# Optimization experiments

Hardware: AMD Instinct MI355X
Metric: run time of the kernel (lower is better)

The kernel has to match this reference:

```python
import jax, jax.numpy as jnp
import numpy as np

EMBED = 256
HEADS = 8
LEVELS = 4
POINTS = 4
HD = EMBED // HEADS  # 32
SHAPES = [(100, 100), (50, 50), (25, 25), (13, 13)]  # (H, W) per level
NV = sum(h * w for h, w in SHAPES)  # 13294
BS = 2


def _lin_params(k, fan_in, fan_out):
    s = 1.0 / np.sqrt(fan_in)
    kw, kb = jax.random.split(k)
    W = jax.random.uniform(kw, (fan_in, fan_out), jnp.float32, -s, s)
    b = jax.random.uniform(kb, (fan_out,), jnp.float32, -s, s)
    return W, b


def setup_inputs():
    key = jax.random.key(0)
    ks = jax.random.split(key, 10)
    inp = {
        "query": jax.random.normal(ks[0], (BS, NV, EMBED), jnp.float32),
        "key": jax.random.normal(ks[1], (BS, NV, EMBED), jnp.float32),
        "value": jax.random.normal(ks[2], (BS, NV, EMBED), jnp.float32),
        "query_pos": jax.random.normal(ks[3], (BS, NV, EMBED), jnp.float32),
        "reference_points": jax.random.uniform(ks[4], (BS, NV, LEVELS, 2), jnp.float32),
        "spatial_shapes": jnp.array(SHAPES, jnp.int32),
        "level_start_index": jnp.array(np.cumsum([0] + [h * w for h, w in SHAPES[:-1]]), jnp.int32),
        "key_padding_mask": jnp.zeros((BS, NV), bool),
    }
    inp["W_value"], inp["b_value"] = _lin_params(ks[5], EMBED, EMBED)
    inp["W_off"], inp["b_off"] = _lin_params(ks[6], EMBED, HEADS * LEVELS * POINTS * 2)
    inp["W_attn"], inp["b_attn"] = _lin_params(ks[7], EMBED, HEADS * LEVELS * POINTS)
    inp["W_out"], inp["b_out"] = _lin_params(ks[8], EMBED, EMBED)
    inp["W_ffn"], inp["b_ffn"] = _lin_params(ks[9], EMBED, EMBED)
    return inp


def _bilinear(v, x, y, H, W):
    # v: (bs, heads, H*W, hd); x, y: (bs, heads, n) pixel coords (align_corners=False)
    # zero padding outside the feature map (matches torch grid_sample padding_mode='zeros')
    x0 = jnp.floor(x)
    y0 = jnp.floor(y)
    lx = x - x0
    ly = y - y0
    x0 = x0.astype(jnp.int32)
    y0 = y0.astype(jnp.int32)

    def g(xi, yi):
        valid = ((xi >= 0) & (xi < W) & (yi >= 0) & (yi < H)).astype(v.dtype)
        idx = jnp.clip(yi, 0, H - 1) * W + jnp.clip(xi, 0, W - 1)
        return jnp.take_along_axis(v, idx[..., None], axis=2) * valid[..., None]

    return (g(x0, y0) * ((1 - lx) * (1 - ly))[..., None]
            + g(x0 + 1, y0) * (lx * (1 - ly))[..., None]
            + g(x0, y0 + 1) * ((1 - lx) * ly)[..., None]
            + g(x0 + 1, y0 + 1) * (lx * ly)[..., None])


def _forward(query, key, value, query_pos, reference_points, shapes, starts,
             key_padding_mask, W_value, b_value, W_off, b_off, W_attn, b_attn,
             W_out, b_out, W_ffn, b_ffn):
    bs, nq, _ = query.shape
    identity = query  # residual taken BEFORE adding positional encoding (mmcv semantics)
    q = query + query_pos
    v = value @ W_value + b_value
    v = jnp.where(key_padding_mask[..., None], 0.0, v).reshape(bs, -1, HEADS, HD)
    off = (q @ W_off + b_off).reshape(bs, nq, HEADS, LEVELS, POINTS, 2)
    aw = jax.nn.softmax((q @ W_attn + b_attn).reshape(bs, nq, HEADS, LEVELS * POINTS), axis=-1)
    aw = aw.reshape(bs, nq, HEADS, LEVELS, POINTS)
    # offset normalizer is (W, H) per level
    wh = jnp.array([[w, h] for h, w in shapes], jnp.float32)
    loc = reference_points[:, :, None, :, None, :] + off / wh[None, None, None, :, None, :]
    out = jnp.zeros((bs, HEADS, nq, HD), q.dtype)
    for l, (H, W) in enumerate(shapes):
        s = starts[l]
        vl = v[:, s:s + H * W].transpose(0, 2, 1, 3)  # (bs, heads, H*W, hd)
        x = (loc[:, :, :, l, :, 0] * W - 0.5).transpose(0, 2, 1, 3).reshape(bs, HEADS, nq * POINTS)
        y = (loc[:, :, :, l, :, 1] * H - 0.5).transpose(0, 2, 1, 3).reshape(bs, HEADS, nq * POINTS)
        smp = _bilinear(vl, x, y, H, W).reshape(bs, HEADS, nq, POINTS, HD)
        wl = aw[:, :, :, l].transpose(0, 2, 1, 3)  # (bs, heads, nq, P)
        out = out + jnp.sum(smp * wl[..., None], axis=3)
    out = out.transpose(0, 2, 1, 3).reshape(bs, nq, EMBED)
    out = out @ W_out + b_out + identity
    return out @ W_ffn + b_ffn


def reference(query, key, value, query_pos, reference_points, spatial_shapes,
              level_start_index, key_padding_mask, W_value, b_value, W_off, b_off,
              W_attn, b_attn, W_out, b_out, W_ffn, b_ffn):
    # spatial shapes / level starts are structural metadata -> treat as static ints
    shapes = [tuple(int(x) for x in r) for r in np.asarray(spatial_shapes)]
    starts = [int(x) for x in np.asarray(level_start_index)]
    return _forward(query, key, value, query_pos, reference_points, shapes, starts,
                    key_padding_mask, W_value, b_value, W_off, b_off, W_attn, b_attn,
                    W_out, b_out, W_ffn, b_ffn)
```

## Files before the change

kernel.cpp:

```cpp
#include <hip/hip_runtime.h>
#include <hip/hip_bf16.h>
#include <math.h>

#define NQ 13294
#define NV 13294
#define M_ROWS (2*NQ)
#define MP 26624

typedef __attribute__((ext_vector_type(8))) short bf16x8;
typedef __attribute__((ext_vector_type(4))) float f32x4;
typedef __attribute__((ext_vector_type(2))) float f32x2;

__device__ __forceinline__ float4 ld4(const float* p){ return *(const float4*)p; }
__device__ __forceinline__ float bfu_lo(unsigned int u){ return __uint_as_float(u << 16); }
__device__ __forceinline__ float bfu_hi(unsigned int u){ return __uint_as_float(u & 0xffff0000u); }
__device__ __forceinline__ f32x2 up2(unsigned int u){
  return (f32x2){__uint_as_float(u << 16), __uint_as_float(u & 0xffff0000u)};
}
__device__ __forceinline__ unsigned short f2bf(float f){
  unsigned int u = __float_as_uint(f);
  u += 0x7fffu + ((u >> 16) & 1u);
  return (unsigned short)(u >> 16);
}
__device__ __forceinline__ unsigned int pk2(float a, float b){
  return (unsigned int)f2bf(a) | ((unsigned int)f2bf(b) << 16);
}
__device__ __forceinline__ void gl_lds16(const unsigned short* g, unsigned short* l) {
  __builtin_amdgcn_global_load_lds(
      (const __attribute__((address_space(1))) unsigned int*)g,
      (__attribute__((address_space(3))) unsigned int*)l, 16, 0, 0);
}

__global__ __launch_bounds__(256) void prep_all(
    const float* __restrict__ value, const float* __restrict__ query,
    const float* __restrict__ qpos,
    unsigned short* __restrict__ val_bf, unsigned short* __restrict__ q_bf,
    const float* __restrict__ wv, const float* __restrict__ wo,
    const float* __restrict__ wa, const float* __restrict__ wu,
    const float* __restrict__ wf, unsigned short* __restrict__ wt)
{
  const int total = MP * 64;
  for (int i = blockIdx.x * 256 + threadIdx.x; i < total; i += gridDim.x * 256) {
    const int e = i * 4;
    ushort4 a = make_ushort4(0,0,0,0), b = make_ushort4(0,0,0,0);
    if (e < M_ROWS * 256) {
      float4 v4 = ld4(value + e);
      a = make_ushort4(f2bf(v4.x), f2bf(v4.y), f2bf(v4.z), f2bf(v4.w));
      float4 q4 = ld4(query + e);
      float4 p4 = ld4(qpos + e);
      b = make_ushort4(f2bf(q4.x+p4.x), f2bf(q4.y+p4.y), f2bf(q4.z+p4.z), f2bf(q4.w+p4.w));
    }
    *(ushort4*)(val_bf + e) = a;
    *(ushort4*)(q_bf   + e) = b;
  }
  for (int t = blockIdx.x * 256 + threadIdx.x; t < 294912; t += gridDim.x * 256) {
    const float* src; int Nn; int base;
    if      (t < 65536)  { src = wv; Nn = 256; base = 0; }
    else if (t < 131072) { src = wo; Nn = 256; base = 65536; }
    else if (t < 163840) { src = wa; Nn = 128; base = 131072; }
    else if (t < 229376) { src = wu; Nn = 256; base = 163840; }
    else                 { src = wf; Nn = 256; base = 229376; }
    const int local = t - base;
    const int n = local >> 8, k = local & 255;
    wt[t] = f2bf(src[k * Nn + n]);
  }
}

template<int NCOL, int OUT_MODE, bool ADD_RES>
__global__ __launch_bounds__(256) void gemm_gl(
    const unsigned short* __restrict__ A, const unsigned short* __restrict__ Bt,
    const float* __restrict__ biasA, const float* __restrict__ biasB,
    const float* __restrict__ RES, void* __restrict__ Cv, int N)
{
  __shared__ unsigned short lds[32768];

  const int nwg = 416 * NCOL;
  const int lin = blockIdx.x;
  const int swz = (lin & 7) * (nwg >> 3) + (lin >> 3);
  const int brow = (swz / NCOL) * 64;
  const int bcol = (swz % NCOL) * 64;

  const int tid  = threadIdx.x;
  const int wid  = tid >> 6, lane = tid & 63;
  const int wr   = wid >> 1, wc = wid & 1;
  const int fr   = lane & 15, fg = lane >> 4;

  {
    const int r0   = lane >> 3;
    const int slot = lane & 7;
    #pragma unroll
    for (int t = 0; t < 4; ++t) {
      #pragma unroll
      for (int c = 0; c < 2; ++c) {
        const int row = (wid * 2 + c) * 8 + r0;
        const int gsl = slot ^ (row & 7);
        gl_lds16(A  + (size_t)(brow + row) * 256 + t * 64 + (gsl << 3),
                 &lds[t * 4096 + (wid * 2 + c) * 512]);
        gl_lds16(Bt + (size_t)(bcol + row) * 256 + t * 64 + (gsl << 3),
                 &lds[16384 + t * 4096 + (wid * 2 + c) * 512]);
      }
    }
  }
  __syncthreads();

  f32x4 acc[2][2];
  #pragma unroll
  for (int m = 0; m < 2; ++m)
    #pragma unroll
    for (int n = 0; n < 2; ++n)
      acc[m][n] = (f32x4){0.f, 0.f, 0.f, 0.f};

  #pragma unroll
  for (int t = 0; t < 4; ++t) {
    const char* as = (const char*)&lds[t * 4096];
    const char* bs = (const char*)&lds[16384 + t * 4096];
    #pragma unroll
    for (int kk = 0; kk < 2; ++kk) {
      const int kb = kk * 64 + fg * 16;
      bf16x8 af[2], bfv[2];
      #pragma unroll
      for (int m = 0; m < 2; ++m) {
        const int r = wr * 32 + m * 16 + fr;
        af[m] = *(const bf16x8*)(as + r * 128 + (kb ^ ((r & 7) << 4)));
      }
      #pragma unroll
      for (int n = 0; n < 2; ++n) {
        const int r = wc * 32 + n * 16 + fr;
        bfv[n] = *(const bf16x8*)(bs + r * 128 + (kb ^ ((r & 7) << 4)));
      }
      #pragma unroll
      for (int m = 0; m < 2; ++m)
        #pragma unroll
        for (int n = 0; n < 2; ++n)
          acc[m][n] = __builtin_amdgcn_mfma_f32_16x16x32_bf16(af[m], bfv[n], acc[m][n], 0, 0, 0);
    }
  }

  __syncthreads();
  float* csh = (float*)lds;
  const int c0 = bcol + wc * 32 + fr;
  const int c1 = c0 + 16;
  const float bn0 = (c0 < 256) ? biasA[c0] : biasB[c0 - 256];
  const float bn1 = (c1 < 256) ? biasA[c1] : biasB[c1 - 256];
  #pragma unroll
  for (int m = 0; m < 2; ++m)
    #pragma unroll
    for (int j = 0; j < 4; ++j) {
      const int row = wr * 32 + m * 16 + fg * 4 + j;
      csh[row * 64 + wc * 32 + fr]      = acc[m][0][j] + bn0;
      csh[row * 64 + wc * 32 + 16 + fr] = acc[m][1][j] + bn1;
    }
  __syncthreads();
  #pragma unroll
  for (int i = 0; i < 4; ++i) {
    const int rl = i * 16 + (tid >> 4);
    const int gr = brow + rl;
    if (gr >= M_ROWS) continue;
    const int c4 = (tid & 15) * 4;
    float4 v = *(const float4*)&csh[rl * 64 + c4];
    if (ADD_RES) {
      float4 q = ld4(RES + (size_t)gr * 256 + bcol + c4);
      v.x += q.x; v.y += q.y; v.z += q.z; v.w += q.w;
    }
    if (OUT_MODE == 0) {
      *(float4*)&((float*)Cv)[(size_t)gr * N + bcol + c4] = v;
    } else if (OUT_MODE == 1) {
      ushort4 pk = make_ushort4(f2bf(v.x), f2bf(v.y), f2bf(v.z), f2bf(v.w));
      *(ushort4*)&((unsigned short*)Cv)[(size_t)gr * N + bcol + c4] = pk;
    } else {
      const int head = (bcol + c4) >> 5;
      const int ch   = c4 & 31;
      ushort4 pk = make_ushort4(f2bf(v.x), f2bf(v.y), f2bf(v.z), f2bf(v.w));
      *(ushort4*)&((unsigned short*)Cv)[((size_t)head * M_ROWS + gr) * 32 + ch] = pk;
    }
  }
}

__global__ __launch_bounds__(256) void msda5(
    const unsigned short* __restrict__ v, const unsigned short* __restrict__ oa,
    const float* __restrict__ ref, unsigned short* __restrict__ attout)
{
  constexpr int LW[4] = {100, 50, 25, 13};
  constexpr int LS[4] = {0, 10000, 12500, 13125};

  __shared__ int4   sidx[64][16];
  __shared__ float4 swt [64][16];

  const int bid   = blockIdx.x;
  const int h     = bid & 7;
  const int chunk = bid >> 3;
  const int tid   = threadIdx.x;
  const int qi    = tid >> 2;
  const int lq    = tid & 3;
  const int bq    = chunk * 64 + qi;
  const bool active = bq < M_ROWS;
  const int b     = (bq >= NQ) ? 1 : 0;
  const int pmask = qi & 7;

  if (active) {
    const int l = lq;
    const int W = LW[l];
    const float fD = (float)W;
    const unsigned short* oarow = oa + (size_t)bq * 384;

    uint2 lg = *(const uint2*)(oarow + 256 + h * 16 + l * 4);
    float g0 = bfu_lo(lg.x), g1 = bfu_hi(lg.x), g2 = bfu_lo(lg.y), g3 = bfu_hi(lg.y);
    float mx = fmaxf(fmaxf(g0, g1), fmaxf(g2, g3));
    mx = fmaxf(mx, __shfl_xor(mx, 1));
    mx = fmaxf(mx, __shfl_xor(mx, 2));
    float e0 = __expf(g0-mx), e1 = __expf(g1-mx), e2 = __expf(g2-mx), e3 = __expf(g3-mx);
    float s = e0 + e1 + e2 + e3;
    s += __shfl_xor(s, 1);
    s += __shfl_xor(s, 2);
    const float inv = 1.f / s;
    const float ee[4] = {e0*inv, e1*inv, e2*inv, e3*inv};

    uint4 ov = *(const uint4*)(oarow + h * 32 + l * 8);
    const float oxy[8] = {bfu_lo(ov.x), bfu_hi(ov.x), bfu_lo(ov.y), bfu_hi(ov.y),
                          bfu_lo(ov.z), bfu_hi(ov.z), bfu_lo(ov.w), bfu_hi(ov.w)};
    const float rx = ref[(size_t)bq * 8 + l * 2];
    const float ry = ref[(size_t)bq * 8 + l * 2 + 1];
    const int rowbase = b * NV + LS[l];

    #pragma unroll
    for (int j = 0; j < 4; ++j) {
      const float x = fmaf(rx, fD, oxy[2*j])   - 0.5f;
      const float y = fmaf(ry, fD, oxy[2*j+1]) - 0.5f;
      const float x0f = floorf(x), y0f = floorf(y);
      const float lx = x - x0f, ly = y - y0f;
      const int x0 = (int)x0f, y0 = (int)y0f;
      const int x1 = x0 + 1,  y1 = y0 + 1;
      const int cx0 = min(max(x0, 0), W - 1), cx1 = min(max(x1, 0), W - 1);
      const int cy0 = min(max(y0, 0), W - 1), cy1 = min(max(y1, 0), W - 1);
      const float f00 = (x0 >= 0 && x0 < W && y0 >= 0 && y0 < W) ? 1.f : 0.f;
      const float f10 = (x1 >= 0 && x1 < W && y0 >= 0 && y0 < W) ? 1.f : 0.f;
      const float f01 = (x0 >= 0 && x0 < W && y1 >= 0 && y1 < W) ? 1.f : 0.f;
      const float f11 = (x1 >= 0 && x1 < W && y1 >= 0 && y1 < W) ? 1.f : 0.f;
      const float wt = ee[j];
      const int pi = (l * 4 + j) ^ pmask;
      sidx[qi][pi] = make_int4((rowbase + cy0 * W + cx0) * 64,
                               (rowbase + cy0 * W + cx1) * 64,
                               (rowbase + cy1 * W + cx0) * 64,
                               (rowbase + cy1 * W + cx1) * 64);
      swt[qi][pi] = make_float4(wt * (1.f - lx) * (1.f - ly) * f00,
                                wt * lx * (1.f - ly) * f10,
                                wt * (1.f - lx) * ly * f01,
                                wt * lx * ly * f11);
    }
  }
  __syncthreads();

  if (active) {
    const char* vb = (const char*)v + (size_t)h * M_ROWS * 64 + lq * 16;
    f32x2 acc2[4];
    #pragma unroll
    for (int k = 0; k < 4; ++k) acc2[k] = (f32x2){0.f, 0.f};
    #pragma unroll
    for (int p = 0; p < 16; ++p) {
      const int4   ix = sidx[qi][p ^ pmask];
      const float4 w4 = swt[qi][p ^ pmask];
      uint4 c0 = *(const uint4*)(vb + ix.x);
      uint4 c1 = *(const uint4*)(vb + ix.y);
      uint4 c2 = *(const uint4*)(vb + ix.z);
      uint4 c3 = *(const uint4*)(vb + ix.w);
      const f32x2 w0 = (f32x2){w4.x, w4.x};
      const f32x2 w1 = (f32x2){w4.y, w4.y};
      const f32x2 w2 = (f32x2){w4.z, w4.z};
      const f32x2 w3 = (f32x2){w4.w, w4.w};
      acc2[0] = w0 * up2(c0.x) + acc2[0];
      acc2[1] = w0 * up2(c0.y) + acc2[1];
      acc2[2] = w0 * up2(c0.z) + acc2[2];
      acc2[3] = w0 * up2(c0.w) + acc2[3];
      acc2[0] = w1 * up2(c1.x) + acc2[0];
      acc2[1] = w1 * up2(c1.y) + acc2[1];
      acc2[2] = w1 * up2(c1.z) + acc2[2];
      acc2[3] = w1 * up2(c1.w) + acc2[3];
      acc2[0] = w2 * up2(c2.x) + acc2[0];
      acc2[1] = w2 * up2(c2.y) + acc2[1];
      acc2[2] = w2 * up2(c2.z) + acc2[2];
      acc2[3] = w2 * up2(c2.w) + acc2[3];
      acc2[0] = w3 * up2(c3.x) + acc2[0];
      acc2[1] = w3 * up2(c3.y) + acc2[1];
      acc2[2] = w3 * up2(c3.z) + acc2[2];
      acc2[3] = w3 * up2(c3.w) + acc2[3];
    }
    uint4 pk;
    pk.x = pk2(acc2[0][0], acc2[0][1]);
    pk.y = pk2(acc2[1][0], acc2[1][1]);
    pk.z = pk2(acc2[2][0], acc2[2][1]);
    pk.w = pk2(acc2[3][0], acc2[3][1]);
    *(uint4*)(attout + (size_t)bq * 256 + h * 32 + lq * 8) = pk;
  }
}

extern "C" void kernel_launch(void* const* d_in, const int* in_sizes, int n_in,
                              void* d_out, int out_size, void* d_ws, size_t ws_size,
                              hipStream_t stream) {
  const float* query  = (const float*)d_in[0];
  const float* value  = (const float*)d_in[2];
  const float* qpos   = (const float*)d_in[3];
  const float* refpts = (const float*)d_in[4];
  const float* W_value = (const float*)d_in[8];
  const float* b_value = (const float*)d_in[9];
  const float* W_off   = (const float*)d_in[10];
  const float* b_off   = (const float*)d_in[11];
  const float* W_attn  = (const float*)d_in[12];
  const float* b_attn  = (const float*)d_in[13];
  const float* W_out   = (const float*)d_in[14];
  const float* b_out   = (const float*)d_in[15];
  const float* W_ffn   = (const float*)d_in[16];
  const float* b_ffn   = (const float*)d_in[17];
  float* out = (float*)d_out;

  unsigned short* oa    = (unsigned short*)d_ws;
  unsigned short* vbuf2 = oa + (size_t)MP * 384;
  unsigned short* AB1   = vbuf2 + (size_t)8 * M_ROWS * 32;
  unsigned short* AB2   = AB1 + (size_t)MP * 256;
  unsigned short* wts   = AB2 + (size_t)MP * 256;
  unsigned short* wv_t  = wts;
  unsigned short* woa_t = wts + 65536;
  unsigned short* wu_t  = wts + 163840;
  unsigned short* wf_t  = wts + 229376;

  const dim3 blk(256);

  prep_all<<<dim3(2048), blk, 0, stream>>>(value, query, qpos, AB1, AB2,
      W_value, W_off, W_attn, W_out, W_ffn, wts);

  gemm_gl<4,2,false><<<dim3(1664), blk, 0, stream>>>(
      AB1, wv_t, b_value, b_value, nullptr, vbuf2, 256);
  gemm_gl<6,1,false><<<dim3(2496), blk, 0, stream>>>(
      AB2, woa_t, b_off, b_attn, nullptr, oa, 384);
  msda5<<<dim3(8 * 416), blk, 0, stream>>>(vbuf2, oa, refpts, AB1);
  gemm_gl<4,1,true><<<dim3(1664), blk, 0, stream>>>(
      AB1, wu_t, b_out, b_out, query, AB2, 256);
  gemm_gl<4,0,false><<<dim3(1664), blk, 0, stream>>>(
      AB2, wf_t, b_ffn, b_ffn, nullptr, (void*)out, 256);
}
```

Measured before the change: 123.2 us.

## Fetch bilinear x-neighbour pairs as one 32-byte row load in sampling kernel

The sampling kernel now uses 8 threads per query instead of 4. Each thread pair covers the two horizontally adjacent corners of a bilinear sample with a single contiguous 16-byte load per row, and edge cases are handled by clamping the x base to W-2 and remapping the corner weights. Per-query gathers drop from four scattered loads to two wider contiguous row segments, and partial sums are combined with a shuffle. The cost is twice as many blocks, half the threads idling at the store, and a new edge-weight remapping that must match zero padding exactly.

```diff
diff --git a/kernel.cpp b/kernel.cpp
--- a/kernel.cpp
+++ b/kernel.cpp
@@ -176,120 +176,115 @@
   }
 }
 
-__global__ __launch_bounds__(256) void msda5(
+__global__ __launch_bounds__(256) void msda6(
     const unsigned short* __restrict__ v, const unsigned short* __restrict__ oa,
     const float* __restrict__ ref, unsigned short* __restrict__ attout)
 {
   constexpr int LW[4] = {100, 50, 25, 13};
   constexpr int LS[4] = {0, 10000, 12500, 13125};
 
-  __shared__ int4   sidx[64][16];
-  __shared__ float4 swt [64][16];
+  __shared__ int2   sidx[32][17];
+  __shared__ float4 swt [32][17];
 
   const int bid   = blockIdx.x;
   const int h     = bid & 7;
   const int chunk = bid >> 3;
   const int tid   = threadIdx.x;
-  const int qi    = tid >> 2;
-  const int lq    = tid & 3;
-  const int bq    = chunk * 64 + qi;
+  const int q     = tid >> 3;
+  const int c     = tid & 7;
+  const int bq    = chunk * 32 + q;
   const bool active = bq < M_ROWS;
   const int b     = (bq >= NQ) ? 1 : 0;
-  const int pmask = qi & 7;
 
   if (active) {
-    const int l = lq;
+    const int l = c >> 1;
     const int W = LW[l];
     const float fD = (float)W;
     const unsigned short* oarow = oa + (size_t)bq * 384;
 
-    uint2 lg = *(const uint2*)(oarow + 256 + h * 16 + l * 4);
-    float g0 = bfu_lo(lg.x), g1 = bfu_hi(lg.x), g2 = bfu_lo(lg.y), g3 = bfu_hi(lg.y);
-    float mx = fmaxf(fmaxf(g0, g1), fmaxf(g2, g3));
+    unsigned int lgu = *(const unsigned int*)(oarow + 256 + h * 16 + c * 2);
+    float g0 = bfu_lo(lgu), g1 = bfu_hi(lgu);
+    float mx = fmaxf(g0, g1);
     mx = fmaxf(mx, __shfl_xor(mx, 1));
     mx = fmaxf(mx, __shfl_xor(mx, 2));
-    float e0 = __expf(g0-mx), e1 = __expf(g1-mx), e2 = __expf(g2-mx), e3 = __expf(g3-mx);
-    float s = e0 + e1 + e2 + e3;
+    mx = fmaxf(mx, __shfl_xor(mx, 4));
+    float e0 = __expf(g0 - mx), e1 = __expf(g1 - mx);
+    float s = e0 + e1;
     s += __shfl_xor(s, 1);
     s += __shfl_xor(s, 2);
+    s += __shfl_xor(s, 4);
     const float inv = 1.f / s;
-    const float ee[4] = {e0*inv, e1*inv, e2*inv, e3*inv};
-
-    uint4 ov = *(const uint4*)(oarow + h * 32 + l * 8);
-    const float oxy[8] = {bfu_lo(ov.x), bfu_hi(ov.x), bfu_lo(ov.y), bfu_hi(ov.y),
-                          bfu_lo(ov.z), bfu_hi(ov.z), bfu_lo(ov.w), bfu_hi(ov.w)};
+    const float wpt[2] = {e0 * inv, e1 * inv};
+
+    uint2 ou = *(const uint2*)(oarow + h * 32 + c * 4);
+    const float oxy[4] = {bfu_lo(ou.x), bfu_hi(ou.x), bfu_lo(ou.y), bfu_hi(ou.y)};
     const float rx = ref[(size_t)bq * 8 + l * 2];
     const float ry = ref[(size_t)bq * 8 + l * 2 + 1];
     const int rowbase = b * NV + LS[l];
 
     #pragma unroll
-    for (int j = 0; j < 4; ++j) {
+    for (int j = 0; j < 2; ++j) {
       const float x = fmaf(rx, fD, oxy[2*j])   - 0.5f;
       const float y = fmaf(ry, fD, oxy[2*j+1]) - 0.5f;
       const float x0f = floorf(x), y0f = floorf(y);
       const float lx = x - x0f, ly = y - y0f;
       const int x0 = (int)x0f, y0 = (int)y0f;
-      const int x1 = x0 + 1,  y1 = y0 + 1;
-      const int cx0 = min(max(x0, 0), W - 1), cx1 = min(max(x1, 0), W - 1);
+      const int y1 = y0 + 1;
+      const int xbase = min(max(x0, 0), W - 2);
+      const float wx0 = 1.f - lx, wx1 = lx;
+      const float we0 = (x0 == xbase     ? wx0 : 0.f) + (x0 == xbase - 1 ? wx1 : 0.f);
+      const float we1 = (x0 == xbase + 1 ? wx0 : 0.f) + (x0 == xbase     ? wx1 : 0.f);
       const int cy0 = min(max(y0, 0), W - 1), cy1 = min(max(y1, 0), W - 1);
-      const float f00 = (x0 >= 0 && x0 < W && y0 >= 0 && y0 < W) ? 1.f : 0.f;
-      const float f10 = (x1 >= 0 && x1 < W && y0 >= 0 && y0 < W) ? 1.f : 0.f;
-      const float f01 = (x0 >= 0 && x0 < W && y1 >= 0 && y1 < W) ? 1.f : 0.f;
-      const float f11 = (x1 >= 0 && x1 < W && y1 >= 0 && y1 < W) ? 1.f : 0.f;
-      const float wt = ee[j];
-      const int pi = (l * 4 + j) ^ pmask;
-      sidx[qi][pi] = make_int4((rowbase + cy0 * W + cx0) * 64,
-                               (rowbase + cy0 * W + cx1) * 64,
-                               (rowbase + cy1 * W + cx0) * 64,
-                               (rowbase + cy1 * W + cx1) * 64);
-      swt[qi][pi] = make_float4(wt * (1.f - lx) * (1.f - ly) * f00,
-                                wt * lx * (1.f - ly) * f10,
-                                wt * (1.f - lx) * ly * f01,
-                                wt * lx * ly * f11);
+      const float wy0 = (y0 >= 0 && y0 < W) ? (1.f - ly) : 0.f;
+      const float wy1 = (y1 >= 0 && y1 < W) ? ly : 0.f;
+      const float wt = wpt[j];
+      const int p = c * 2 + j;
+      sidx[q][p] = make_int2((rowbase + cy0 * W + xbase) * 64,
+                             (rowbase + cy1 * W + xbase) * 64);
+      swt[q][p] = make_float4(wt * wy0 * we0, wt * wy0 * we1,
+                              wt * wy1 * we0, wt * wy1 * we1);
     }
   }
   __syncthreads();
 
   if (active) {
-    const char* vb = (const char*)v + (size_t)h * M_ROWS * 64 + lq * 16;
+    const char* vb = (const char*)v + (size_t)h * M_ROWS * 64 + c * 16;
+    const int el = c >> 2;
     f32x2 acc2[4];
     #pragma unroll
     for (int k = 0; k < 4; ++k) acc2[k] = (f32x2){0.f, 0.f};
     #pragma unroll
     for (int p = 0; p < 16; ++p) {
-      const int4   ix = sidx[qi][p ^ pmask];
-      const float4 w4 = swt[qi][p ^ pmask];
-      uint4 c0 = *(const uint4*)(vb + ix.x);
-      uint4 c1 = *(const uint4*)(vb + ix.y);
-      uint4 c2 = *(const uint4*)(vb + ix.z);
-      uint4 c3 = *(const uint4*)(vb + ix.w);
-      const f32x2 w0 = (f32x2){w4.x, w4.x};
-      const f32x2 w1 = (f32x2){w4.y, w4.y};
-      const f32x2 w2 = (f32x2){w4.z, w4.z};
-      const f32x2 w3 = (f32x2){w4.w, w4.w};
-      acc2[0] = w0 * up2(c0.x) + acc2[0];
-      acc2[1] = w0 * up2(c0.y) + acc2[1];
-      acc2[2] = w0 * up2(c0.z) + acc2[2];
-      acc2[3] = w0 * up2(c0.w) + acc2[3];
-      acc2[0] = w1 * up2(c1.x) + acc2[0];
-      acc2[1] = w1 * up2(c1.y) + acc2[1];
-      acc2[2] = w1 * up2(c1.z) + acc2[2];
-      acc2[3] = w1 * up2(c1.w) + acc2[3];
-      acc2[0] = w2 * up2(c2.x) + acc2[0];
-      acc2[1] = w2 * up2(c2.y) + acc2[1];
-      acc2[2] = w2 * up2(c2.z) + acc2[2];
-      acc2[3] = w2 * up2(c2.w) + acc2[3];
-      acc2[0] = w3 * up2(c3.x) + acc2[0];
-      acc2[1] = w3 * up2(c3.y) + acc2[1];
-      acc2[2] = w3 * up2(c3.z) + acc2[2];
-      acc2[3] = w3 * up2(c3.w) + acc2[3];
-    }
-    uint4 pk;
-    pk.x = pk2(acc2[0][0], acc2[0][1]);
-    pk.y = pk2(acc2[1][0], acc2[1][1]);
-    pk.z = pk2(acc2[2][0], acc2[2][1]);
-    pk.w = pk2(acc2[3][0], acc2[3][1]);
-    *(uint4*)(attout + (size_t)bq * 256 + h * 32 + lq * 8) = pk;
+      const int2   ix = sidx[q][p];
+      const float4 w4 = swt[q][p];
+      uint4 r0 = *(const uint4*)(vb + ix.x);
+      uint4 r1 = *(const uint4*)(vb + ix.y);
+      const float wa = el ? w4.y : w4.x;
+      const float wb = el ? w4.w : w4.z;
+      const f32x2 wav = (f32x2){wa, wa};
+      const f32x2 wbv = (f32x2){wb, wb};
+      acc2[0] = wav * up2(r0.x) + acc2[0];
+      acc2[1] = wav * up2(r0.y) + acc2[1];
+      acc2[2] = wav * up2(r0.z) + acc2[2];
+      acc2[3] = wav * up2(r0.w) + acc2[3];
+      acc2[0] = wbv * up2(r1.x) + acc2[0];
+      acc2[1] = wbv * up2(r1.y) + acc2[1];
+      acc2[2] = wbv * up2(r1.z) + acc2[2];
+      acc2[3] = wbv * up2(r1.w) + acc2[3];
+    }
+    #pragma unroll
+    for (int k = 0; k < 4; ++k) {
+      acc2[k][0] += __shfl_xor(acc2[k][0], 4);
+      acc2[k][1] += __shfl_xor(acc2[k][1], 4);
+    }
+    if (c < 4) {
+      uint4 pk;
+      pk.x = pk2(acc2[0][0], acc2[0][1]);
+      pk.y = pk2(acc2[1][0], acc2[1][1]);
+      pk.z = pk2(acc2[2][0], acc2[2][1]);
+      pk.w = pk2(acc2[3][0], acc2[3][1]);
+      *(uint4*)(attout + (size_t)bq * 256 + h * 32 + c * 8) = pk;
+    }
   }
 }
 
@@ -331,7 +326,7 @@
       AB1, wv_t, b_value, b_value, nullptr, vbuf2, 256);
   gemm_gl<6,1,false><<<dim3(2496), blk, 0, stream>>>(
       AB2, woa_t, b_off, b_attn, nullptr, oa, 384);
-  msda5<<<dim3(8 * 416), blk, 0, stream>>>(vbuf2, oa, refpts, AB1);
+  msda6<<<dim3(8 * 831), blk, 0, stream>>>(vbuf2, oa, refpts, AB1);
   gemm_gl<4,1,true><<<dim3(1664), blk, 0, stream>>>(
       AB1, wu_t, b_out, b_out, query, AB2, 256);
   gemm_gl<4,0,false><<<dim3(1664), blk, 0, stream>>>(
```

Measured after the change: 120.9 us. About the same (-1.8%).
